# Kernel tuning notes

Measured on AMD Instinct MI355X. Metric: run time of the kernel, lower is better.

The kernel has to match this reference:

```python
import jax, jax.numpy as jnp
import numpy as np

B, S, E, H = 64, 100, 512, 1024  # H must equal 2*E (bmm in attention)
VS, VT, P = 32000, 32000, 100


def setup_inputs() -> dict:
    key = jax.random.key(0)
    ks = jax.random.split(key, 16)
    sc = 0.02
    return {
        "source_sentences": jax.random.randint(ks[0], (B, S), 0, VS),
        "positions": jax.random.randint(ks[1], (B, S), 0, P),
        "target_words": jax.random.randint(ks[2], (B,), 0, VT),
        "source_lengths": jnp.full((B,), S, dtype=jnp.int64 if jax.config.jax_enable_x64 else jnp.int32),
        "max_len": S,
        "emb_in": jax.random.normal(ks[3], (VS, E), jnp.float32) * sc,
        "emb_out": jax.random.normal(ks[4], (VT, E), jnp.float32) * sc,
        "emb_pos": jax.random.normal(ks[5], (P, E), jnp.float32) * sc,
        "W_scale": jax.random.normal(ks[6], (H, 2 * E), jnp.float32) * sc,
        "b_scale": jnp.zeros((H,), jnp.float32),
        "W_ih": jax.random.normal(ks[7], (H, E + H), jnp.float32) * sc,
        "b_ih": jnp.zeros((H,), jnp.float32),
        "W_hh": jax.random.normal(ks[8], (H, H), jnp.float32) * sc,
        "b_hh": jnp.zeros((H,), jnp.float32),
        "W_proj": jax.random.normal(ks[9], (VT, H), jnp.float32) * sc,
        "b_proj": jnp.zeros((VT,), jnp.float32),
    }


def reference(source_sentences, positions, target_words, source_lengths, max_len,
              emb_in, emb_out, emb_pos, W_scale, b_scale,
              W_ih, b_ih, W_hh, b_hh, W_proj, b_proj):
    # --- encoder_forward ---
    words = emb_in[source_sentences]              # [B,S,E]
    pos = emb_pos[positions]                      # [B,S,E]
    enc = jnp.concatenate([words, pos], axis=-1)  # [B,S,2E] combined embeddings
    h0 = jnp.mean(enc, axis=1) @ W_scale.T + b_scale  # [B,H]
    # --- attention (vectorized form of the per-position bmm loop) ---
    energy = jnp.einsum('bh,bsh->bs', h0, enc)        # [B,S]
    align = jax.nn.softmax(energy, axis=1)            # softmax over source positions
    # original uses torch.mean (not sum) over positions
    context = jnp.mean(align[:, :, None] * enc, axis=1)  # [B,2E] == [B,H]
    # --- decoder step ---
    out_w = emb_out[target_words]                      # [B,E]
    x = jnp.concatenate([out_w, context], axis=-1)     # [B,E+H]
    # nn.RNN single step, tanh nonlinearity
    h = jnp.tanh(x @ W_ih.T + b_ih + h0 @ W_hh.T + b_hh)  # [B,H]
    out = h @ W_proj.T + b_proj                        # [B,VT]
    return (out, h)
```

## Files before the change

kernel.cpp:

```cpp
#include <hip/hip_runtime.h>

typedef __attribute__((ext_vector_type(8))) __bf16 bf16x8;
typedef __attribute__((ext_vector_type(4))) float  f32x4;
typedef unsigned short u16;

__device__ __forceinline__ u16 f2bf(float f) {
    union { float f; unsigned int i; } v; v.f = f;
    unsigned int r = v.i + 0x7fffu + ((v.i >> 16) & 1u);
    return (u16)(r >> 16);
}
__device__ __forceinline__ unsigned pack2(float a, float b) {
    union { float f; unsigned u; } x, y; x.f = a; y.f = b;
    return __builtin_amdgcn_perm(y.u + 0x8000u, x.u + 0x8000u, 0x07060302u);
}

#define B_  64
#define S_  100
#define E_  512
#define H_  1024
#define VT_ 32000
#define Kc  128
#define PITCH 128

__global__ __launch_bounds__(256, 1)
void k1_encmean(const int* __restrict__ src, const int* __restrict__ pos,
                const float* __restrict__ emb_in, const float* __restrict__ emb_pos,
                u16* __restrict__ encmean) {
    int b = blockIdx.x, q4 = blockIdx.y, t = threadIdx.x;
    __shared__ int sidx[S_], pidx[S_];
    __shared__ float part[256][4];
    if (t < S_) { sidx[t] = src[b * S_ + t]; pidx[t] = pos[b * S_ + t]; }
    __syncthreads();

    int f4 = t & 63, g = t >> 6;
    bool isPos = (q4 >= 2);
    const float* base = isPos ? emb_pos : emb_in;
    const int*   idx  = isPos ? pidx : sidx;
    int col = (q4 & 1) * 256 + f4 * 4;

    float a0 = 0.f, a1 = 0.f, a2 = 0.f, a3 = 0.f;
    int s0 = g * 25;
    #pragma unroll 5
    for (int s = s0; s < s0 + 25; s++) {
        const float4 v = *(const float4*)(base + (size_t)idx[s] * E_ + col);
        a0 += v.x; a1 += v.y; a2 += v.z; a3 += v.w;
    }
    part[t][0] = a0; part[t][1] = a1; part[t][2] = a2; part[t][3] = a3;
    __syncthreads();

    if (t < 64) {
        const float inv = 1.0f / (float)S_;
        float r0 = 0.f, r1 = 0.f, r2 = 0.f, r3 = 0.f;
        #pragma unroll
        for (int g2 = 0; g2 < 4; g2++) {
            r0 += part[g2 * 64 + t][0]; r1 += part[g2 * 64 + t][1];
            r2 += part[g2 * 64 + t][2]; r3 += part[g2 * 64 + t][3];
        }
        int e = q4 * 256 + t * 4;
        u16* o = encmean + (size_t)b * (2 * E_) + e;
        o[0] = f2bf(r0 * inv); o[1] = f2bf(r1 * inv);
        o[2] = f2bf(r2 * inv); o[3] = f2bf(r3 * inv);
    }
}

#define MFMA16(a, bfrag, c) __builtin_amdgcn_mfma_f32_16x16x32_bf16((a), (bfrag), (c), 0, 0, 0)

template<int KLEN, int LDA, int LDW>
__device__ __forceinline__ void gemm_lds(const u16* __restrict__ A,
                                         const float* __restrict__ W,
                                         int jt, int koff, u16* __restrict__ ldsW,
                                         f32x4 acc[4], int t) {
    constexpr int NC = KLEN / Kc;
    const int lane = t & 63, w = t >> 6, m = lane & 15, q = lane >> 4;
    const int r = t >> 2, c4 = t & 3;
    const float* wsrc = W + (size_t)(jt + r) * LDW + koff + c4 * 4;
    const u16*   arow = A + (size_t)(w * 16 + m) * LDA + koff + q * 8;
    const int halfoff = (c4 & 1) * 4;

    float4 v[8];
    #pragma unroll
    for (int i = 0; i < 8; i++) v[i] = *(const float4*)(wsrc + i * 16);
    #pragma unroll
    for (int i = 0; i < 8; i++) {
        int U = (c4 >> 1) + 2 * i;
        uint2 p; p.x = pack2(v[i].x, v[i].y); p.y = pack2(v[i].z, v[i].w);
        *(uint2*)(ldsW + r * PITCH + ((U ^ (r & 15)) * 8) + halfoff) = p;
    }
    __syncthreads();

    for (int c = 0; c < NC; c++) {
        if (c + 1 < NC) {
            #pragma unroll
            for (int i = 0; i < 8; i++)
                v[i] = *(const float4*)(wsrc + (c + 1) * Kc + i * 16);
        }
        const u16* lb = ldsW + (c & 1) * (64 * PITCH);
        const u16* ar = arow + c * Kc;
        #pragma unroll
        for (int ks = 0; ks < 4; ks++) {
            bf16x8 a = *(const bf16x8*)(ar + ks * 32);
            #pragma unroll
            for (int f = 0; f < 4; f++) {
                int rr = f * 16 + m;
                int U  = ks * 4 + q;
                bf16x8 bfr = *(const bf16x8*)(lb + rr * PITCH + ((U ^ (rr & 15)) * 8));
                acc[f] = MFMA16(a, bfr, acc[f]);
            }
        }
        if (c + 1 < NC) {
            u16* wd = ldsW + ((c + 1) & 1) * (64 * PITCH) + r * PITCH;
            #pragma unroll
            for (int i = 0; i < 8; i++) {
                int U = (c4 >> 1) + 2 * i;
                uint2 p; p.x = pack2(v[i].x, v[i].y); p.y = pack2(v[i].z, v[i].w);
                *(uint2*)(wd + ((U ^ (r & 15)) * 8) + halfoff) = p;
            }
        }
        __syncthreads();
    }
}

__global__ __launch_bounds__(256, 2)
void k2_h0p(const u16* __restrict__ encmean, const float* __restrict__ Wscale,
            float* __restrict__ part2) {
    __shared__ u16 ldsW[2 * 64 * PITCH];
    int t = threadIdx.x, lane = t & 63, w = t >> 6, m = lane & 15, q = lane >> 4;
    int jt = blockIdx.x * 64, sp = blockIdx.y;
    f32x4 acc[4] = {{0,0,0,0},{0,0,0,0},{0,0,0,0},{0,0,0,0}};
    gemm_lds<256, 2 * E_, 2 * E_>(encmean, Wscale, jt, sp * 256, ldsW, acc, t);
    #pragma unroll
    for (int f = 0; f < 4; f++) {
        int j = jt + 16 * f + m;
        #pragma unroll
        for (int r2 = 0; r2 < 4; r2++) {
            int bb = w * 16 + q * 4 + r2;
            part2[(size_t)(sp * B_ + bb) * H_ + j] = acc[f][r2];
        }
    }
}

__global__ __launch_bounds__(256, 1)
void k3_attn(const int* __restrict__ src, const int* __restrict__ pos,
             const int* __restrict__ tgt,
             const float* __restrict__ emb_in, const float* __restrict__ emb_pos,
             const float* __restrict__ emb_out,
             const float* __restrict__ part2, const float* __restrict__ bscale,
             u16* __restrict__ x, u16* __restrict__ h0b) {
    int b = blockIdx.x, t = threadIdx.x;
    __shared__ float h0s[2 * E_];
    __shared__ int sidx[S_], pidx[S_];
    __shared__ float energy[S_];
    __shared__ float align_s[S_];

    for (int i = t; i < 2 * E_; i += 256) {
        float v = bscale[i];
        #pragma unroll
        for (int ks = 0; ks < 4; ks++) v += part2[(size_t)(ks * B_ + b) * H_ + i];
        h0s[i] = v;
        h0b[(size_t)b * H_ + i] = f2bf(v);
    }
    if (t < S_) { sidx[t] = src[b * S_ + t]; pidx[t] = pos[b * S_ + t]; }
    __syncthreads();

    int lane = t & 63, w = t >> 6;
    for (int s = w; s < S_; s += 4) {
        const float* ri = emb_in  + (size_t)sidx[s] * E_;
        const float* rp = emb_pos + (size_t)pidx[s] * E_;
        float acc = 0.f;
        #pragma unroll
        for (int ii = 0; ii < 8; ii++) { int k = lane + 64 * ii; acc += ri[k] * h0s[k]; }
        #pragma unroll
        for (int ii = 0; ii < 8; ii++) { int k = lane + 64 * ii; acc += rp[k] * h0s[E_ + k]; }
        #pragma unroll
        for (int off = 32; off; off >>= 1) acc += __shfl_down(acc, off);
        if (lane == 0) energy[s] = acc;
    }
    __syncthreads();

    if (t < 64) {
        float e0 = energy[t];
        float e1 = (t + 64 < S_) ? energy[t + 64] : -1e30f;
        float mx = fmaxf(e0, e1);
        #pragma unroll
        for (int off = 32; off; off >>= 1) mx = fmaxf(mx, __shfl_xor(mx, off));
        float p0 = expf(e0 - mx);
        float p1 = (t + 64 < S_) ? expf(e1 - mx) : 0.f;
        float ss = p0 + p1;
        #pragma unroll
        for (int off = 32; off; off >>= 1) ss += __shfl_xor(ss, off);
        float inv = 1.0f / (ss * (float)S_);
        align_s[t] = p0 * inv;
        if (t + 64 < S_) align_s[t + 64] = p1 * inv;
    }
    __syncthreads();

    if (t < 128) {
        int o = t;
        bool isPos = (o >= 64);
        const float* base = isPos ? emb_pos : emb_in;
        const int* idx  = isPos ? pidx : sidx;
        int eo = (o & 63) * 8;
        float c[8] = {0,0,0,0,0,0,0,0};
        for (int s = 0; s < S_; s++) {
            const float* row = base + (size_t)idx[s] * E_ + eo;
            float al = align_s[s];
            const float4 v0 = *(const float4*)(row);
            const float4 v1 = *(const float4*)(row + 4);
            c[0] += al * v0.x; c[1] += al * v0.y; c[2] += al * v0.z; c[3] += al * v0.w;
            c[4] += al * v1.x; c[5] += al * v1.y; c[6] += al * v1.z; c[7] += al * v1.w;
        }
        u16* xo = x + (size_t)b * (E_ + H_) + E_ + o * 8;
        #pragma unroll
        for (int i = 0; i < 8; i++) xo[i] = f2bf(c[i]);
    } else {
        int i = t - 128;
        int tw = tgt[b];
        const float4 v = *((const float4*)(emb_out + (size_t)tw * E_) + i);
        ushort4 o; o.x = f2bf(v.x); o.y = f2bf(v.y); o.z = f2bf(v.z); o.w = f2bf(v.w);
        *((ushort4*)(x + (size_t)b * (E_ + H_)) + i) = o;
    }
}

__global__ __launch_bounds__(256, 2)
void k4_hp(const u16* __restrict__ xb, const float* __restrict__ Wih,
           const u16* __restrict__ h0b, const float* __restrict__ Whh,
           float* __restrict__ part4) {
    __shared__ u16 ldsW[2 * 64 * PITCH];
    int t = threadIdx.x, lane = t & 63, w = t >> 6, m = lane & 15, q = lane >> 4;
    int jt = blockIdx.x * 64, sp = blockIdx.y;
    f32x4 acc[4] = {{0,0,0,0},{0,0,0,0},{0,0,0,0},{0,0,0,0}};
    if (sp < 6) gemm_lds<256, E_ + H_, E_ + H_>(xb,  Wih, jt, sp * 256,       ldsW, acc, t);
    else        gemm_lds<256, H_,      H_     >(h0b, Whh, jt, (sp - 6) * 256, ldsW, acc, t);
    #pragma unroll
    for (int f = 0; f < 4; f++) {
        int j = jt + 16 * f + m;
        #pragma unroll
        for (int r2 = 0; r2 < 4; r2++) {
            int bb = w * 16 + q * 4 + r2;
            part4[(size_t)(sp * B_ + bb) * H_ + j] = acc[f][r2];
        }
    }
}

__global__ __launch_bounds__(256, 1)
void k4_red(const float* __restrict__ part4,
            const float* __restrict__ bih, const float* __restrict__ bhh,
            float* __restrict__ houtf, u16* __restrict__ hbf) {
    int b = blockIdx.x, t = threadIdx.x;
    int j = t * 4;
    float4 s  = *(const float4*)(bih + j);
    const float4 b2 = *(const float4*)(bhh + j);
    s.x += b2.x; s.y += b2.y; s.z += b2.z; s.w += b2.w;
    #pragma unroll
    for (int ks = 0; ks < 10; ks++) {
        const float4 p = *(const float4*)(part4 + (size_t)(ks * B_ + b) * H_ + j);
        s.x += p.x; s.y += p.y; s.z += p.z; s.w += p.w;
    }
    float4 h; h.x = tanhf(s.x); h.y = tanhf(s.y); h.z = tanhf(s.z); h.w = tanhf(s.w);
    *(float4*)(houtf + (size_t)b * H_ + j) = h;
    ushort4 o; o.x = f2bf(h.x); o.y = f2bf(h.y); o.z = f2bf(h.z); o.w = f2bf(h.w);
    *(ushort4*)(hbf + (size_t)b * H_ + j) = o;
}

__global__ __launch_bounds__(256, 2)
void k5_out(const u16* __restrict__ hb, const float* __restrict__ Wp,
            const float* __restrict__ bp, float* __restrict__ out) {
    __shared__ u16 ldsW[2 * 64 * PITCH];
    int t = threadIdx.x, lane = t & 63, w = t >> 6, m = lane & 15, q = lane >> 4;
    int jt = blockIdx.x * 64;
    f32x4 acc[4] = {{0,0,0,0},{0,0,0,0},{0,0,0,0},{0,0,0,0}};
    gemm_lds<H_, H_, H_>(hb, Wp, jt, 0, ldsW, acc, t);
    #pragma unroll
    for (int f = 0; f < 4; f++) {
        int j = jt + 16 * f + m;
        float bias = bp[j];
        #pragma unroll
        for (int r = 0; r < 4; r++) {
            int b = w * 16 + q * 4 + r;
            out[(size_t)b * VT_ + j] = acc[f][r] + bias;
        }
    }
}

extern "C" void kernel_launch(void* const* d_in, const int* in_sizes, int n_in,
                              void* d_out, int out_size, void* d_ws, size_t ws_size,
                              hipStream_t stream) {
    const int*   src     = (const int*)d_in[0];
    const int*   pos     = (const int*)d_in[1];
    const int*   tgt     = (const int*)d_in[2];
    const float* emb_in  = (const float*)d_in[5];
    const float* emb_out = (const float*)d_in[6];
    const float* emb_pos = (const float*)d_in[7];
    const float* Wscale  = (const float*)d_in[8];
    const float* bscale  = (const float*)d_in[9];
    const float* Wih     = (const float*)d_in[10];
    const float* bih     = (const float*)d_in[11];
    const float* Whh     = (const float*)d_in[12];
    const float* bhh     = (const float*)d_in[13];
    const float* Wproj   = (const float*)d_in[14];
    const float* bproj   = (const float*)d_in[15];

    char* ws = (char*)d_ws;
    u16*   encmean = (u16*)(ws);
    u16*   xb      = (u16*)(ws + 131072);
    u16*   h0b     = (u16*)(ws + 327680);
    u16*   hbf     = (u16*)(ws + 458752);
    float* part2   = (float*)(ws + 589824);
    float* part4   = (float*)(ws + 1638400);

    float* out   = (float*)d_out;
    float* houtf = out + (size_t)B_ * VT_;

    hipLaunchKernelGGL(k1_encmean, dim3(B_, 4),      dim3(256), 0, stream,
                       src, pos, emb_in, emb_pos, encmean);
    hipLaunchKernelGGL(k2_h0p,     dim3(H_ / 64, 4), dim3(256), 0, stream,
                       encmean, Wscale, part2);
    hipLaunchKernelGGL(k3_attn,    dim3(B_),         dim3(256), 0, stream,
                       src, pos, tgt, emb_in, emb_pos, emb_out, part2, bscale, xb, h0b);
    hipLaunchKernelGGL(k4_hp,      dim3(H_ / 64, 10), dim3(256), 0, stream,
                       xb, Wih, h0b, Whh, part4);
    hipLaunchKernelGGL(k4_red,     dim3(B_),         dim3(256), 0, stream,
                       part4, bih, bhh, houtf, hbf);
    hipLaunchKernelGGL(k5_out,     dim3(VT_ / 64),   dim3(256), 0, stream,
                       hbf, Wproj, bproj, out);
}
```

Baseline: 322.0 us.

## Double split-K for h0 and RNN GEMMs and fuse reduction via last-block atomic

Halves the K chunk per block in the h0 and RNN-step GEMMs, doubling the split-K grid so more CUs are busy on these small-batch matmuls. Removes the separate k4_red launch: each k4_hp block bumps a per-column-tile atomic counter, and the last block to finish sums the partials, applies bias and tanh, and writes h. The counter is reset in k3_attn. This saves one launch and raises parallelism, at the cost of more partial-sum traffic and a serialized tail reduction in one block per tile.

```diff
diff --git a/kernel.cpp b/kernel.cpp
--- a/kernel.cpp
+++ b/kernel.cpp
@@ -21,6 +21,8 @@
 #define VT_ 32000
 #define Kc  128
 #define PITCH 128
+#define NS2 8
+#define NS4 20
 
 __global__ __launch_bounds__(256, 1)
 void k1_encmean(const int* __restrict__ src, const int* __restrict__ pos,
@@ -123,11 +125,11 @@
 __global__ __launch_bounds__(256, 2)
 void k2_h0p(const u16* __restrict__ encmean, const float* __restrict__ Wscale,
             float* __restrict__ part2) {
-    __shared__ u16 ldsW[2 * 64 * PITCH];
+    __shared__ u16 ldsW[64 * PITCH];
     int t = threadIdx.x, lane = t & 63, w = t >> 6, m = lane & 15, q = lane >> 4;
     int jt = blockIdx.x * 64, sp = blockIdx.y;
     f32x4 acc[4] = {{0,0,0,0},{0,0,0,0},{0,0,0,0},{0,0,0,0}};
-    gemm_lds<256, 2 * E_, 2 * E_>(encmean, Wscale, jt, sp * 256, ldsW, acc, t);
+    gemm_lds<Kc, 2 * E_, 2 * E_>(encmean, Wscale, jt, sp * Kc, ldsW, acc, t);
     #pragma unroll
     for (int f = 0; f < 4; f++) {
         int j = jt + 16 * f + m;
@@ -145,17 +147,20 @@
              const float* __restrict__ emb_in, const float* __restrict__ emb_pos,
              const float* __restrict__ emb_out,
              const float* __restrict__ part2, const float* __restrict__ bscale,
-             u16* __restrict__ x, u16* __restrict__ h0b) {
+             u16* __restrict__ x, u16* __restrict__ h0b,
+             unsigned* __restrict__ cnt4) {
     int b = blockIdx.x, t = threadIdx.x;
     __shared__ float h0s[2 * E_];
     __shared__ int sidx[S_], pidx[S_];
     __shared__ float energy[S_];
     __shared__ float align_s[S_];
 
+    if (b == 0 && t < 16) cnt4[t] = 0;
+
     for (int i = t; i < 2 * E_; i += 256) {
         float v = bscale[i];
         #pragma unroll
-        for (int ks = 0; ks < 4; ks++) v += part2[(size_t)(ks * B_ + b) * H_ + i];
+        for (int ks = 0; ks < NS2; ks++) v += part2[(size_t)(ks * B_ + b) * H_ + i];
         h0s[i] = v;
         h0b[(size_t)b * H_ + i] = f2bf(v);
     }
@@ -224,13 +229,16 @@
 __global__ __launch_bounds__(256, 2)
 void k4_hp(const u16* __restrict__ xb, const float* __restrict__ Wih,
            const u16* __restrict__ h0b, const float* __restrict__ Whh,
-           float* __restrict__ part4) {
-    __shared__ u16 ldsW[2 * 64 * PITCH];
+           const float* __restrict__ bih, const float* __restrict__ bhh,
+           float* __restrict__ part4, unsigned* __restrict__ cnt4,
+           float* __restrict__ houtf, u16* __restrict__ hbf) {
+    __shared__ u16 ldsW[64 * PITCH];
+    __shared__ int lastflag;
     int t = threadIdx.x, lane = t & 63, w = t >> 6, m = lane & 15, q = lane >> 4;
     int jt = blockIdx.x * 64, sp = blockIdx.y;
     f32x4 acc[4] = {{0,0,0,0},{0,0,0,0},{0,0,0,0},{0,0,0,0}};
-    if (sp < 6) gemm_lds<256, E_ + H_, E_ + H_>(xb,  Wih, jt, sp * 256,       ldsW, acc, t);
-    else        gemm_lds<256, H_,      H_     >(h0b, Whh, jt, (sp - 6) * 256, ldsW, acc, t);
+    if (sp < 12) gemm_lds<Kc, E_ + H_, E_ + H_>(xb,  Wih, jt, sp * Kc,        ldsW, acc, t);
+    else         gemm_lds<Kc, H_,      H_     >(h0b, Whh, jt, (sp - 12) * Kc, ldsW, acc, t);
     #pragma unroll
     for (int f = 0; f < 4; f++) {
         int j = jt + 16 * f + m;
@@ -240,26 +248,29 @@
             part4[(size_t)(sp * B_ + bb) * H_ + j] = acc[f][r2];
         }
     }
-}
-
-__global__ __launch_bounds__(256, 1)
-void k4_red(const float* __restrict__ part4,
-            const float* __restrict__ bih, const float* __restrict__ bhh,
-            float* __restrict__ houtf, u16* __restrict__ hbf) {
-    int b = blockIdx.x, t = threadIdx.x;
-    int j = t * 4;
-    float4 s  = *(const float4*)(bih + j);
-    const float4 b2 = *(const float4*)(bhh + j);
-    s.x += b2.x; s.y += b2.y; s.z += b2.z; s.w += b2.w;
-    #pragma unroll
-    for (int ks = 0; ks < 10; ks++) {
-        const float4 p = *(const float4*)(part4 + (size_t)(ks * B_ + b) * H_ + j);
-        s.x += p.x; s.y += p.y; s.z += p.z; s.w += p.w;
-    }
-    float4 h; h.x = tanhf(s.x); h.y = tanhf(s.y); h.z = tanhf(s.z); h.w = tanhf(s.w);
-    *(float4*)(houtf + (size_t)b * H_ + j) = h;
-    ushort4 o; o.x = f2bf(h.x); o.y = f2bf(h.y); o.z = f2bf(h.z); o.w = f2bf(h.w);
-    *(ushort4*)(hbf + (size_t)b * H_ + j) = o;
+    __threadfence();
+    __syncthreads();
+    if (t == 0) lastflag = (atomicAdd(&cnt4[blockIdx.x], 1u) == NS4 - 1);
+    __syncthreads();
+    if (lastflag) {
+        __threadfence();
+        int jj = jt + (t & 15) * 4;
+        int b0 = (t >> 4) * 4;
+        for (int bb = b0; bb < b0 + 4; bb++) {
+            float4 s  = *(const float4*)(bih + jj);
+            const float4 b2 = *(const float4*)(bhh + jj);
+            s.x += b2.x; s.y += b2.y; s.z += b2.z; s.w += b2.w;
+            #pragma unroll
+            for (int ks = 0; ks < NS4; ks++) {
+                const float4 p = *(const float4*)(part4 + (size_t)(ks * B_ + bb) * H_ + jj);
+                s.x += p.x; s.y += p.y; s.z += p.z; s.w += p.w;
+            }
+            float4 h; h.x = tanhf(s.x); h.y = tanhf(s.y); h.z = tanhf(s.z); h.w = tanhf(s.w);
+            *(float4*)(houtf + (size_t)bb * H_ + jj) = h;
+            ushort4 o; o.x = f2bf(h.x); o.y = f2bf(h.y); o.z = f2bf(h.z); o.w = f2bf(h.w);
+            *(ushort4*)(hbf + (size_t)bb * H_ + jj) = o;
+        }
+    }
 }
 
 __global__ __launch_bounds__(256, 2)
@@ -301,26 +312,26 @@
     const float* bproj   = (const float*)d_in[15];
 
     char* ws = (char*)d_ws;
-    u16*   encmean = (u16*)(ws);
-    u16*   xb      = (u16*)(ws + 131072);
-    u16*   h0b     = (u16*)(ws + 327680);
-    u16*   hbf     = (u16*)(ws + 458752);
-    float* part2   = (float*)(ws + 589824);
-    float* part4   = (float*)(ws + 1638400);
+    u16*      encmean = (u16*)(ws);
+    u16*      xb      = (u16*)(ws + 131072);
+    u16*      h0b     = (u16*)(ws + 327680);
+    u16*      hbf     = (u16*)(ws + 458752);
+    unsigned* cnt4    = (unsigned*)(ws + 589824);
+    float*    part2   = (float*)(ws + 590848);
+    float*    part4   = (float*)(ws + 2688000);
 
     float* out   = (float*)d_out;
     float* houtf = out + (size_t)B_ * VT_;
 
-    hipLaunchKernelGGL(k1_encmean, dim3(B_, 4),      dim3(256), 0, stream,
+    hipLaunchKernelGGL(k1_encmean, dim3(B_, 4),        dim3(256), 0, stream,
                        src, pos, emb_in, emb_pos, encmean);
-    hipLaunchKernelGGL(k2_h0p,     dim3(H_ / 64, 4), dim3(256), 0, stream,
+    hipLaunchKernelGGL(k2_h0p,     dim3(H_ / 64, NS2), dim3(256), 0, stream,
                        encmean, Wscale, part2);
-    hipLaunchKernelGGL(k3_attn,    dim3(B_),         dim3(256), 0, stream,
-                       src, pos, tgt, emb_in, emb_pos, emb_out, part2, bscale, xb, h0b);
-    hipLaunchKernelGGL(k4_hp,      dim3(H_ / 64, 10), dim3(256), 0, stream,
-                       xb, Wih, h0b, Whh, part4);
-    hipLaunchKernelGGL(k4_red,     dim3(B_),         dim3(256), 0, stream,
-                       part4, bih, bhh, houtf, hbf);
-    hipLaunchKernelGGL(k5_out,     dim3(VT_ / 64),   dim3(256), 0, stream,
+    hipLaunchKernelGGL(k3_attn,    dim3(B_),           dim3(256), 0, stream,
+                       src, pos, tgt, emb_in, emb_pos, emb_out, part2, bscale,
+                       xb, h0b, cnt4);
+    hipLaunchKernelGGL(k4_hp,      dim3(H_ / 64, NS4), dim3(256), 0, stream,
+                       xb, Wih, h0b, Whh, bih, bhh, part4, cnt4, houtf, hbf);
+    hipLaunchKernelGGL(k5_out,     dim3(VT_ / 64),     dim3(256), 0, stream,
                        hbf, Wproj, bproj, out);
 }
```

Result: slower. 360.0 us (+11.8%).
